# Performance work log

Measured on AMD Instinct MI355X. Metric: run time of the kernel, lower is better.

## Reference

```python
import jax, jax.numpy as jnp
import numpy as np

N_NODES = 50000
N_EDGES = 800000
D_IN = 128
D_OUT = 128
N_MLP = 2


def _lin(x, W, b):
    return x @ W.T + b


def setup_inputs() -> dict:
    key = jax.random.key(0)
    ks = jax.random.split(key, 32)
    d = {}
    d['feat'] = jax.random.normal(ks[0], (N_NODES, D_IN), dtype=jnp.float32)
    d['src'] = jax.random.randint(ks[1], (N_EDGES,), 0, N_NODES, dtype=jnp.int32)
    d['dst'] = jax.random.randint(ks[2], (N_EDGES,), 0, N_NODES, dtype=jnp.int32)
    s_in = 1.0 / np.sqrt(D_IN)
    s_out = 1.0 / np.sqrt(D_OUT)
    i = 3
    def w(shape, s):
        nonlocal i
        out = jax.random.normal(ks[i], shape, dtype=jnp.float32) * s
        i += 1
        return out
    for nm in ['asrc', 'adst', 'asub', 'amul']:
        d['W_' + nm] = w((D_OUT, D_IN), s_in)
        d['b_' + nm] = w((D_OUT,), s_in)
    d['W_aout'] = w((1, D_OUT), s_out)
    d['b_aout'] = w((1,), s_out)
    for nm in ['pool', 'pool2']:
        d['W_' + nm] = w((D_IN, D_IN), s_in)
        d['b_' + nm] = w((D_IN,), s_in)
    for nm in ['self', 'neigh', 'neigh2']:
        d['W_' + nm] = w((D_OUT, D_IN), s_in)
        d['b_' + nm] = w((D_OUT,), s_in)
    d['W_mlp'] = w((N_MLP, D_OUT, D_OUT), s_out)
    d['b_mlp'] = w((N_MLP, D_OUT), s_out)
    return d


def reference(feat, src, dst,
              W_asrc, b_asrc, W_adst, b_adst, W_asub, b_asub, W_amul, b_amul,
              W_aout, b_aout, W_pool, b_pool, W_pool2, b_pool2,
              W_self, b_self, W_neigh, b_neigh, W_neigh2, b_neigh2,
              W_mlp, b_mlp):
    gelu = lambda x: jax.nn.gelu(x, approximate=False)
    fs = feat[src]            # [E, D_IN] gathered source feats
    fd = feat[dst]            # [E, D_IN] gathered dest feats
    # edge attention score
    e = _lin(fs - fd, W_asub, b_asub) + _lin(fs * fd, W_amul, b_amul)
    e = e + _lin(feat, W_asrc, b_asrc)[src] + _lin(feat, W_adst, b_adst)[dst]
    e = gelu(e)
    e = jax.nn.leaky_relu(_lin(e, W_aout, b_aout), 0.2)  # [E, 1]
    deg = jax.ops.segment_sum(jnp.ones((src.shape[0],), jnp.float32), dst,
                              num_segments=N_NODES)      # in-degree
    has_in = (deg > 0)[:, None]
    # max-pool branch
    h = gelu(_lin(feat, W_pool, b_pool))
    m = e * h[src]
    neigh = jax.ops.segment_max(m, dst, num_segments=N_NODES)
    neigh = jnp.where(has_in, neigh, 0.0)
    # mean-pool branch
    h2 = gelu(_lin(feat, W_pool2, b_pool2))
    m2 = e * h2[src]
    neigh2 = jax.ops.segment_sum(m2, dst, num_segments=N_NODES)
    neigh2 = neigh2 / jnp.maximum(deg, 1.0)[:, None]
    rst = _lin(feat, W_self, b_self) + _lin(neigh, W_neigh, b_neigh) \
        + _lin(neigh2, W_neigh2, b_neigh2)
    for li in range(W_mlp.shape[0]):
        rst = rst + _lin(gelu(rst), W_mlp[li], b_mlp[li])
    return rst
```

## Files before the change

kernel.cpp:

```cpp
#include <hip/hip_runtime.h>
#include <cstdint>
#include <cstddef>

#define NN 50000
#define NE 800000
#define DD 128

static_assert(NN % 16 == 0, "node tiles");
static_assert(NE % 16 == 0, "edge tiles");

typedef __bf16 bf16_t;
typedef bf16_t bf16x8 __attribute__((ext_vector_type(8)));
typedef bf16_t bf16x4 __attribute__((ext_vector_type(4)));
typedef bf16_t bf16x2 __attribute__((ext_vector_type(2)));
typedef float f32x4 __attribute__((ext_vector_type(4)));
typedef float f32x16 __attribute__((ext_vector_type(16)));

__device__ __forceinline__ float gelu_f(float x) {
    float u = x * x;
    float t = fmaf(u, -0.1029442445f, -2.3021184019f);
    float s = __builtin_amdgcn_exp2f(x * t);
    return x * __builtin_amdgcn_rcpf(1.0f + s);
}

__device__ __forceinline__ int frag_idx(int ch, int k) {
    int t = ch >> 4, n = ch & 15;
    int kb = k >> 5, r = k & 31, q = r >> 3, j = r & 7;
    return ((((t * 4 + kb) * 4 + q) * 16 + n) << 3) + j;
}

__device__ __forceinline__ int frag32_idx(int ch, int k) {
    int t = ch >> 5, m = ch & 31;
    int kc = k >> 4, q = (k >> 3) & 1, j = k & 7;
    return ((((t * 8 + kc) * 2 + q) * 32 + m) << 3) + j;
}

__global__ __launch_bounds__(256) void convert_feat_kernel(
    const float* __restrict__ feat, bf16_t* __restrict__ fb,
    const int* __restrict__ dst, int* __restrict__ deg)
{
    int i = blockIdx.x * 256 + threadIdx.x;
    f32x4 v = ((const f32x4*)feat)[i];
    bf16x4 o;
    o[0] = (bf16_t)v[0]; o[1] = (bf16_t)v[1]; o[2] = (bf16_t)v[2]; o[3] = (bf16_t)v[3];
    ((bf16x4*)fb)[i] = o;
    if (i < NE) atomicAdd(&deg[dst[i]], 1);
}

__global__ __launch_bounds__(256) void prep_kernel(
    const float* __restrict__ W_asrc, const float* __restrict__ b_asrc,
    const float* __restrict__ W_adst, const float* __restrict__ b_adst,
    const float* __restrict__ W_asub, const float* __restrict__ b_asub,
    const float* __restrict__ W_amul, const float* __restrict__ b_amul,
    const float* __restrict__ W_pool, const float* __restrict__ W_pool2,
    const float* __restrict__ W_self, const float* __restrict__ b_self,
    const float* __restrict__ W_neigh, const float* __restrict__ b_neigh,
    const float* __restrict__ W_neigh2, const float* __restrict__ b_neigh2,
    const float* __restrict__ W_mlp,
    bf16_t* __restrict__ W_Sf, bf16_t* __restrict__ W_Df, bf16_t* __restrict__ W_amulf,
    bf16_t* __restrict__ W_poolf, bf16_t* __restrict__ W_pool2f,
    bf16_t* __restrict__ W_selff, bf16_t* __restrict__ W_neighf, bf16_t* __restrict__ W_neigh2f,
    bf16_t* __restrict__ W_mlpf,
    float* __restrict__ b_e, float* __restrict__ b_rst)
{
    int gid = blockIdx.x * 256 + threadIdx.x;
    float sub = W_asub[gid];
    int ch = gid >> 7, k = gid & 127;
    int fi = frag_idx(ch, k);
    W_Sf[fi] = (bf16_t)(W_asrc[gid] + sub);
    W_Df[fi] = (bf16_t)(W_adst[gid] - sub);
    W_amulf[frag32_idx(ch, k)] = (bf16_t)W_amul[gid];
    W_poolf[fi]   = (bf16_t)W_pool[gid];
    W_pool2f[fi]  = (bf16_t)W_pool2[gid];
    W_selff[fi]   = (bf16_t)W_self[gid];
    W_neighf[fi]  = (bf16_t)W_neigh[gid];
    W_neigh2f[fi] = (bf16_t)W_neigh2[gid];
    W_mlpf[fi]            = (bf16_t)W_mlp[gid];
    W_mlpf[DD * DD + fi]  = (bf16_t)W_mlp[DD * DD + gid];
    if (gid < DD) {
        b_e[gid]   = b_asub[gid] + b_amul[gid] + b_asrc[gid] + b_adst[gid];
        b_rst[gid] = b_self[gid] + b_neigh[gid] + b_neigh2[gid];
    }
}

__device__ __forceinline__ void mm16_store_ilv(
    const bf16x8 a[4], const bf16_t* __restrict__ Wf, const float* __restrict__ bias,
    bf16_t* __restrict__ hh, int nb, int n, int q, int lane, int sub)
{
#pragma unroll
    for (int t = 0; t < 8; t++) {
        f32x4 acc = {0.f, 0.f, 0.f, 0.f};
#pragma unroll
        for (int kb = 0; kb < 4; kb++) {
            bf16x8 b = *(const bf16x8*)(Wf + (((t * 4 + kb) * 64 + lane) << 3));
            acc = __builtin_amdgcn_mfma_f32_16x16x32_bf16(a[kb], b, acc, 0, 0, 0);
        }
        int ch = t * 16 + n;
        int pos = ((ch >> 1) << 2) + (ch & 1) + sub;
        float bv = bias[ch];
#pragma unroll
        for (int r = 0; r < 4; r++)
            hh[(size_t)(nb + q * 4 + r) * 256 + pos] = (bf16_t)gelu_f(acc[r] + bv);
    }
}

__device__ __forceinline__ void mm16_store_plain(
    const bf16x8 a[4], const bf16_t* __restrict__ Wf, const float* __restrict__ bias,
    bf16_t* __restrict__ out, int nb, int n, int q, int lane)
{
#pragma unroll
    for (int t = 0; t < 8; t++) {
        f32x4 acc = {0.f, 0.f, 0.f, 0.f};
#pragma unroll
        for (int kb = 0; kb < 4; kb++) {
            bf16x8 b = *(const bf16x8*)(Wf + (((t * 4 + kb) * 64 + lane) << 3));
            acc = __builtin_amdgcn_mfma_f32_16x16x32_bf16(a[kb], b, acc, 0, 0, 0);
        }
        int ch = t * 16 + n;
        float bv = bias ? bias[ch] : 0.0f;
#pragma unroll
        for (int r = 0; r < 4; r++)
            out[(size_t)(nb + q * 4 + r) * DD + ch] = (bf16_t)(acc[r] + bv);
    }
}

__global__ __launch_bounds__(256) void node_linear_kernel(
    const bf16_t* __restrict__ fb,
    const bf16_t* __restrict__ W_poolf, const float* __restrict__ b_pool,
    const bf16_t* __restrict__ W_pool2f, const float* __restrict__ b_pool2,
    const bf16_t* __restrict__ W_Sf, const float* __restrict__ b_e,
    const bf16_t* __restrict__ W_Df,
    bf16_t* __restrict__ hh, bf16_t* __restrict__ us, bf16_t* __restrict__ ud)
{
    int wid = blockIdx.x * 4 + (threadIdx.x >> 6);
    if (wid >= NN / 16) return;
    int lane = threadIdx.x & 63, n = lane & 15, q = lane >> 4;
    int nb = wid * 16;
    bf16x8 a[4];
#pragma unroll
    for (int kb = 0; kb < 4; kb++)
        a[kb] = *(const bf16x8*)(fb + (size_t)(nb + n) * DD + kb * 32 + q * 8);
    mm16_store_ilv(a, W_poolf, b_pool, hh, nb, n, q, lane, 0);
    mm16_store_ilv(a, W_pool2f, b_pool2, hh, nb, n, q, lane, 2);
    mm16_store_plain(a, W_Sf, b_e, us, nb, n, q, lane);
    mm16_store_plain(a, W_Df, nullptr, ud, nb, n, q, lane);
}

#define SCAN_NB ((NN + 255) / 256)

__global__ __launch_bounds__(256) void scan1_kernel(const int* __restrict__ deg,
                                                    int* __restrict__ offsets, int* __restrict__ bsum)
{
    __shared__ int tmp[256];
    int t = threadIdx.x, g = blockIdx.x * 256 + t;
    int v = (g < NN) ? deg[g] : 0;
    tmp[t] = v;
    __syncthreads();
#pragma unroll
    for (int d = 1; d < 256; d <<= 1) {
        int x = (t >= d) ? tmp[t - d] : 0;
        __syncthreads();
        tmp[t] += x;
        __syncthreads();
    }
    if (g < NN) offsets[g] = tmp[t] - v;
    if (t == 255) bsum[blockIdx.x] = tmp[255];
}

__global__ __launch_bounds__(256) void scan2_kernel(const int* __restrict__ bsum, int* __restrict__ bbase)
{
    __shared__ int tmp[256];
    int t = threadIdx.x;
    int v = (t < SCAN_NB) ? bsum[t] : 0;
    tmp[t] = v;
    __syncthreads();
#pragma unroll
    for (int d = 1; d < 256; d <<= 1) {
        int x = (t >= d) ? tmp[t - d] : 0;
        __syncthreads();
        tmp[t] += x;
        __syncthreads();
    }
    if (t < SCAN_NB) bbase[t] = tmp[t] - v;
}

__global__ __launch_bounds__(256) void scan3_kernel(const int* __restrict__ bbase,
                                                    int* __restrict__ offsets, int* __restrict__ cursor)
{
    int g = blockIdx.x * 256 + threadIdx.x;
    if (g < NN) {
        int o = offsets[g] + bbase[blockIdx.x];
        offsets[g] = o;
        cursor[g] = o;
    }
}

#define ES_NBLK 2500
#define ES_ITERS (NE / 32 / ES_NBLK)

__global__ __launch_bounds__(256, 4) void edge_score_kernel(
    const bf16_t* __restrict__ fb, const int* __restrict__ src, const int* __restrict__ dst,
    const bf16_t* __restrict__ us, const bf16_t* __restrict__ ud,
    const bf16_t* __restrict__ W_amulf,
    const float* __restrict__ w_aout, const float* __restrict__ b_aout,
    int* __restrict__ cursor, int2* __restrict__ csr)
{
    __shared__ __align__(16) bf16_t sP[2][32 * 128];
    __shared__ __align__(16) bf16_t sU[2][32 * 128];
    __shared__ float partials[32 * 5];
    __shared__ float sWa[128];
    int tid = threadIdx.x;
    int wave = tid >> 6, lane = tid & 63;
    int n = lane & 31, q = lane >> 5;
    int t = wave;

    if (tid < 128) sWa[tid] = w_aout[tid];

    bf16x8 wAm[8];
#pragma unroll
    for (int kc = 0; kc < 8; kc++)
        wAm[kc] = *(const bf16x8*)(W_amulf + ((((t * 8 + kc) * 2 + q) * 32 + n) << 3));
    float bout = b_aout[0];

    int sed0 = tid >> 4, sc = tid & 15;

    int e0 = blockIdx.x * 32;
    int s0 = src[e0 + sed0],      d0 = dst[e0 + sed0];
    int s1 = src[e0 + sed0 + 16], d1 = dst[e0 + sed0 + 16];
    bf16x8 pfs0 = *(const bf16x8*)(fb + (size_t)s0 * DD + sc * 8);
    bf16x8 pfd0 = *(const bf16x8*)(fb + (size_t)d0 * DD + sc * 8);
    bf16x8 pus0 = *(const bf16x8*)(us + (size_t)s0 * DD + sc * 8);
    bf16x8 pud0 = *(const bf16x8*)(ud + (size_t)d0 * DD + sc * 8);
    bf16x8 pfs1 = *(const bf16x8*)(fb + (size_t)s1 * DD + sc * 8);
    bf16x8 pfd1 = *(const bf16x8*)(fb + (size_t)d1 * DD + sc * 8);
    bf16x8 pus1 = *(const bf16x8*)(us + (size_t)s1 * DD + sc * 8);
    bf16x8 pud1 = *(const bf16x8*)(ud + (size_t)d1 * DD + sc * 8);

    for (int it = 0; it < ES_ITERS; it++) {
        int buf = it & 1;
        int eb = (blockIdx.x + it * ES_NBLK) * 32;
        {
            bf16x8 pp, uu;
#pragma unroll
            for (int j = 0; j < 8; j++) {
                pp[j] = (bf16_t)((float)pfs0[j] * (float)pfd0[j]);
                uu[j] = (bf16_t)((float)pus0[j] + (float)pud0[j]);
            }
            int ph = (sc ^ (sed0 & 7)) << 3;
            *(bf16x8*)(sP[buf] + sed0 * 128 + ph) = pp;
            *(bf16x8*)(sU[buf] + sed0 * 128 + ph) = uu;
        }
        {
            int ed = sed0 + 16;
            bf16x8 pp, uu;
#pragma unroll
            for (int j = 0; j < 8; j++) {
                pp[j] = (bf16_t)((float)pfs1[j] * (float)pfd1[j]);
                uu[j] = (bf16_t)((float)pus1[j] + (float)pud1[j]);
            }
            int ph = (sc ^ (ed & 7)) << 3;
            *(bf16x8*)(sP[buf] + ed * 128 + ph) = pp;
            *(bf16x8*)(sU[buf] + ed * 128 + ph) = uu;
        }
        __syncthreads();
        if (it + 1 < ES_ITERS) {
            int e1 = (blockIdx.x + (it + 1) * ES_NBLK) * 32;
            s0 = src[e1 + sed0];      d0 = dst[e1 + sed0];
            s1 = src[e1 + sed0 + 16]; d1 = dst[e1 + sed0 + 16];
            pfs0 = *(const bf16x8*)(fb + (size_t)s0 * DD + sc * 8);
            pfd0 = *(const bf16x8*)(fb + (size_t)d0 * DD + sc * 8);
            pus0 = *(const bf16x8*)(us + (size_t)s0 * DD + sc * 8);
            pud0 = *(const bf16x8*)(ud + (size_t)d0 * DD + sc * 8);
            pfs1 = *(const bf16x8*)(fb + (size_t)s1 * DD + sc * 8);
            pfd1 = *(const bf16x8*)(fb + (size_t)d1 * DD + sc * 8);
            pus1 = *(const bf16x8*)(us + (size_t)s1 * DD + sc * 8);
            pud1 = *(const bf16x8*)(ud + (size_t)d1 * DD + sc * 8);
        }
        f32x16 acc = {};
        int swz = n & 7;
#pragma unroll
        for (int kc = 0; kc < 8; kc++) {
            bf16x8 bP = *(const bf16x8*)(sP[buf] + n * 128 + (((kc * 2 + q) ^ swz) << 3));
            acc = __builtin_amdgcn_mfma_f32_32x32x16_bf16(wAm[kc], bP, acc, 0, 0, 0);
        }
        float psum = 0.f;
#pragma unroll
        for (int c = 0; c < 4; c++) {
            bf16x4 sv = *(const bf16x4*)(sU[buf] + n * 128 + (((t * 4 + c) ^ swz) << 3) + q * 4);
            f32x4 wv = *(const f32x4*)(sWa + t * 32 + c * 8 + q * 4);
#pragma unroll
            for (int j = 0; j < 4; j++)
                psum = fmaf(gelu_f(acc[c * 4 + j] + (float)sv[j]), wv[j], psum);
        }
        psum += __shfl_xor(psum, 32, 64);
        if (lane < 32) partials[lane * 5 + wave] = psum;
        __syncthreads();
        if (wave == (it & 3) && lane < 32) {
            int e = eb + lane;
            const float* pr = partials + lane * 5;
            float s = pr[0] + pr[1] + pr[2] + pr[3] + bout;
            s = s > 0.f ? s : 0.2f * s;
            int d = dst[e];
            int pos = atomicAdd(&cursor[d], 1);
            int2 pk;
            pk.x = src[e];
            pk.y = __float_as_int(s);
            csr[pos] = pk;
        }
    }
}

__global__ __launch_bounds__(256) void aggregate_kernel(
    const bf16_t* __restrict__ hh,
    const int* __restrict__ offsets, const int* __restrict__ cursor_end,
    const int2* __restrict__ csr,
    bf16_t* __restrict__ neigh, bf16_t* __restrict__ neigh2)
{
    int wave = threadIdx.x >> 6, lane = threadIdx.x & 63;
    int v = blockIdx.x * 4 + wave;
    if (v >= NN) return;
    int off = offsets[v];
    int dg = cursor_end[v] - off;
    int quarter = lane >> 4;
    int cl = lane & 15;
    float mx[8], sm[8];
#pragma unroll
    for (int j = 0; j < 8; j++) { mx[j] = -INFINITY; sm[j] = 0.f; }
    for (int base = 0; base < dg; base += 64) {
        int cnt = dg - base; if (cnt > 64) cnt = 64;
        int s_l = 0; float sc_l = 0.f;
        if (lane < cnt) {
            int2 pk = csr[off + base + lane];
            s_l = pk.x;
            sc_l = __int_as_float(pk.y);
        }
        int nit = (cnt + 3) >> 2;
#pragma unroll 2
        for (int i = 0; i < nit; i++) {
            int idx = 4 * i + quarter;
            int s = __shfl(s_l, idx, 64);
            float sc = __shfl(sc_l, idx, 64);
            if (idx < cnt) {
                const bf16_t* row = hh + (size_t)s * 256 + 16 * cl;
                bf16x8 h0 = *(const bf16x8*)(row);
                bf16x8 h1 = *(const bf16x8*)(row + 8);
                mx[0] = fmaxf(mx[0], sc * (float)h0[0]);
                mx[1] = fmaxf(mx[1], sc * (float)h0[1]);
                sm[0] = fmaf(sc, (float)h0[2], sm[0]);
                sm[1] = fmaf(sc, (float)h0[3], sm[1]);
                mx[2] = fmaxf(mx[2], sc * (float)h0[4]);
                mx[3] = fmaxf(mx[3], sc * (float)h0[5]);
                sm[2] = fmaf(sc, (float)h0[6], sm[2]);
                sm[3] = fmaf(sc, (float)h0[7], sm[3]);
                mx[4] = fmaxf(mx[4], sc * (float)h1[0]);
                mx[5] = fmaxf(mx[5], sc * (float)h1[1]);
                sm[4] = fmaf(sc, (float)h1[2], sm[4]);
                sm[5] = fmaf(sc, (float)h1[3], sm[5]);
                mx[6] = fmaxf(mx[6], sc * (float)h1[4]);
                mx[7] = fmaxf(mx[7], sc * (float)h1[5]);
                sm[6] = fmaf(sc, (float)h1[6], sm[6]);
                sm[7] = fmaf(sc, (float)h1[7], sm[7]);
            }
        }
    }
#pragma unroll
    for (int j = 0; j < 8; j++) {
        mx[j] = fmaxf(mx[j], __shfl_xor(mx[j], 16, 64));
        mx[j] = fmaxf(mx[j], __shfl_xor(mx[j], 32, 64));
        sm[j] += __shfl_xor(sm[j], 16, 64);
        sm[j] += __shfl_xor(sm[j], 32, 64);
    }
    if (quarter == 0) {
        float inv = 1.0f / (float)(dg > 1 ? dg : 1);
        bf16x8 n1, n2;
#pragma unroll
        for (int j = 0; j < 8; j++) {
            n1[j] = (bf16_t)(dg > 0 ? mx[j] : 0.0f);
            n2[j] = (bf16_t)(sm[j] * inv);
        }
        *(bf16x8*)(neigh + (size_t)v * DD + 8 * cl) = n1;
        *(bf16x8*)(neigh2 + (size_t)v * DD + 8 * cl) = n2;
    }
}

__global__ __launch_bounds__(256) void final_kernel(
    const bf16_t* __restrict__ fb, const bf16_t* __restrict__ neigh, const bf16_t* __restrict__ neigh2,
    const bf16_t* __restrict__ W_selff, const bf16_t* __restrict__ W_neighf, const bf16_t* __restrict__ W_neigh2f,
    const float* __restrict__ b_rst,
    const bf16_t* __restrict__ W_mlpf, const float* __restrict__ b_mlp,
    float* __restrict__ out)
{
    __shared__ __align__(16) float lds[4][16 * 132];
    int wave = threadIdx.x >> 6;
    int wid = blockIdx.x * 4 + wave;
    if (wid >= NN / 16) return;
    int lane = threadIdx.x & 63, n = lane & 15, q = lane >> 4;
    int nb = wid * 16;
    float* L = lds[wave];

    bf16x8 af[4], an[4], am[4];
#pragma unroll
    for (int kb = 0; kb < 4; kb++) {
        size_t o = (size_t)(nb + n) * DD + kb * 32 + q * 8;
        af[kb] = *(const bf16x8*)(fb + o);
        an[kb] = *(const bf16x8*)(neigh + o);
        am[kb] = *(const bf16x8*)(neigh2 + o);
    }
    f32x4 rst[8];
#pragma unroll
    for (int t = 0; t < 8; t++) {
        f32x4 acc = {0.f, 0.f, 0.f, 0.f};
#pragma unroll
        for (int kb = 0; kb < 4; kb++) {
            int wo = ((t * 4 + kb) * 64 + lane) << 3;
            acc = __builtin_amdgcn_mfma_f32_16x16x32_bf16(af[kb], *(const bf16x8*)(W_selff + wo), acc, 0, 0, 0);
            acc = __builtin_amdgcn_mfma_f32_16x16x32_bf16(an[kb], *(const bf16x8*)(W_neighf + wo), acc, 0, 0, 0);
            acc = __builtin_amdgcn_mfma_f32_16x16x32_bf16(am[kb], *(const bf16x8*)(W_neigh2f + wo), acc, 0, 0, 0);
        }
        float bv = b_rst[t * 16 + n];
#pragma unroll
        for (int r = 0; r < 4; r++) acc[r] += bv;
        rst[t] = acc;
    }

#pragma unroll
    for (int li = 0; li < 2; li++) {
#pragma unroll
        for (int t = 0; t < 8; t++)
#pragma unroll
            for (int r = 0; r < 4; r++)
                L[(q * 4 + r) * 132 + t * 16 + n] = gelu_f(rst[t][r]);
        __builtin_amdgcn_wave_barrier();
        bf16x8 g[4];
#pragma unroll
        for (int kb = 0; kb < 4; kb++) {
            const f32x4* p = (const f32x4*)&L[n * 132 + kb * 32 + q * 8];
            f32x4 x0 = p[0], x1 = p[1];
            bf16x8 gg;
            gg[0] = (bf16_t)x0[0]; gg[1] = (bf16_t)x0[1]; gg[2] = (bf16_t)x0[2]; gg[3] = (bf16_t)x0[3];
            gg[4] = (bf16_t)x1[0]; gg[5] = (bf16_t)x1[1]; gg[6] = (bf16_t)x1[2]; gg[7] = (bf16_t)x1[3];
            g[kb] = gg;
        }
        __builtin_amdgcn_wave_barrier();
        const bf16_t* Wl = W_mlpf + li * DD * DD;
#pragma unroll
        for (int t = 0; t < 8; t++) {
            f32x4 acc = {0.f, 0.f, 0.f, 0.f};
#pragma unroll
            for (int kb = 0; kb < 4; kb++) {
                bf16x8 b = *(const bf16x8*)(Wl + (((t * 4 + kb) * 64 + lane) << 3));
                acc = __builtin_amdgcn_mfma_f32_16x16x32_bf16(g[kb], b, acc, 0, 0, 0);
            }
            float bm = b_mlp[li * DD + t * 16 + n];
#pragma unroll
            for (int r = 0; r < 4; r++) rst[t][r] += acc[r] + bm;
        }
    }

#pragma unroll
    for (int t = 0; t < 8; t++)
#pragma unroll
        for (int r = 0; r < 4; r++)
            out[(size_t)(nb + q * 4 + r) * DD + t * 16 + n] = rst[t][r];
}

extern "C" void kernel_launch(void* const* d_in, const int* in_sizes, int n_in,
                              void* d_out, int out_size, void* d_ws, size_t ws_size,
                              hipStream_t stream)
{
    const float* feat    = (const float*)d_in[0];
    const int*   src     = (const int*)d_in[1];
    const int*   dst     = (const int*)d_in[2];
    const float* W_asrc  = (const float*)d_in[3],  *b_asrc  = (const float*)d_in[4];
    const float* W_adst  = (const float*)d_in[5],  *b_adst  = (const float*)d_in[6];
    const float* W_asub  = (const float*)d_in[7],  *b_asub  = (const float*)d_in[8];
    const float* W_amul  = (const float*)d_in[9],  *b_amul  = (const float*)d_in[10];
    const float* W_aout  = (const float*)d_in[11], *b_aout  = (const float*)d_in[12];
    const float* W_pool  = (const float*)d_in[13], *b_pool  = (const float*)d_in[14];
    const float* W_pool2 = (const float*)d_in[15], *b_pool2 = (const float*)d_in[16];
    const float* W_self  = (const float*)d_in[17], *b_self  = (const float*)d_in[18];
    const float* W_neigh = (const float*)d_in[19], *b_neigh = (const float*)d_in[20];
    const float* W_neigh2= (const float*)d_in[21], *b_neigh2= (const float*)d_in[22];
    const float* W_mlp   = (const float*)d_in[23], *b_mlp   = (const float*)d_in[24];
    float* out = (float*)d_out;

    char* w = (char*)d_ws;
    auto take = [&](size_t bytes) -> void* {
        void* p = (void*)w;
        w += (bytes + 255) & ~(size_t)255;
        return p;
    };
    bf16_t* fb      = (bf16_t*)take((size_t)NN * DD * sizeof(bf16_t));
    bf16_t* neigh   = (bf16_t*)take((size_t)NN * DD * sizeof(bf16_t));
    bf16_t* neigh2  = (bf16_t*)take((size_t)NN * DD * sizeof(bf16_t));
    bf16_t* hh      = (bf16_t*)take((size_t)NN * 256 * sizeof(bf16_t));
    bf16_t* us      = (bf16_t*)take((size_t)NN * DD * sizeof(bf16_t));
    bf16_t* ud      = (bf16_t*)take((size_t)NN * DD * sizeof(bf16_t));
    int*    deg     = (int*)take((size_t)NN * sizeof(int));
    int*    offsets = (int*)take((size_t)NN * sizeof(int));
    int*    cursor  = (int*)take((size_t)NN * sizeof(int));
    int2*   csr     = (int2*)take((size_t)NE * sizeof(int2));
    int*    bsum    = (int*)take(256 * sizeof(int));
    int*    bbase   = (int*)take(256 * sizeof(int));
    bf16_t* W_Sf    = (bf16_t*)take((size_t)DD * DD * sizeof(bf16_t));
    bf16_t* W_Df    = (bf16_t*)take((size_t)DD * DD * sizeof(bf16_t));
    bf16_t* W_amulf = (bf16_t*)take((size_t)DD * DD * sizeof(bf16_t));
    bf16_t* W_poolf = (bf16_t*)take((size_t)DD * DD * sizeof(bf16_t));
    bf16_t* W_pool2f= (bf16_t*)take((size_t)DD * DD * sizeof(bf16_t));
    bf16_t* W_selff = (bf16_t*)take((size_t)DD * DD * sizeof(bf16_t));
    bf16_t* W_neighf= (bf16_t*)take((size_t)DD * DD * sizeof(bf16_t));
    bf16_t* W_neigh2f=(bf16_t*)take((size_t)DD * DD * sizeof(bf16_t));
    bf16_t* W_mlpf  = (bf16_t*)take((size_t)2 * DD * DD * sizeof(bf16_t));
    float*  b_e     = (float*)take((size_t)DD * sizeof(float));
    float*  b_rst   = (float*)take((size_t)DD * sizeof(float));

    (void)hipMemsetAsync(deg, 0, (size_t)NN * sizeof(int), stream);

    convert_feat_kernel<<<NN * DD / 4 / 256, 256, 0, stream>>>(feat, fb, dst, deg);

    prep_kernel<<<DD * DD / 256, 256, 0, stream>>>(
        W_asrc, b_asrc, W_adst, b_adst, W_asub, b_asub, W_amul, b_amul,
        W_pool, W_pool2, W_self, b_self, W_neigh, b_neigh, W_neigh2, b_neigh2, W_mlp,
        W_Sf, W_Df, W_amulf, W_poolf, W_pool2f, W_selff, W_neighf, W_neigh2f, W_mlpf,
        b_e, b_rst);

    const int nwaves = NN / 16;
    const int ngrid = (nwaves + 3) / 4;
    node_linear_kernel<<<ngrid, 256, 0, stream>>>(
        fb, W_poolf, b_pool, W_pool2f, b_pool2, W_Sf, b_e, W_Df, hh, us, ud);

    scan1_kernel<<<SCAN_NB, 256, 0, stream>>>(deg, offsets, bsum);
    scan2_kernel<<<1, 256, 0, stream>>>(bsum, bbase);
    scan3_kernel<<<SCAN_NB, 256, 0, stream>>>(bbase, offsets, cursor);

    edge_score_kernel<<<ES_NBLK, 256, 0, stream>>>(
        fb, src, dst, us, ud, W_amulf, W_aout, b_aout, cursor, csr);

    aggregate_kernel<<<(NN + 3) / 4, 256, 0, stream>>>(
        hh, offsets, cursor, csr, neigh, neigh2);

    final_kernel<<<ngrid, 256, 0, stream>>>(
        fb, neigh, neigh2, W_selff, W_neighf, W_neigh2f, b_rst, W_mlpf, b_mlp, out);
}
```

Before: 425.8 us.

## Sort edges by destination before scoring so edge gathers hit dst-sorted order

```diff
diff --git a/kernel.cpp b/kernel.cpp
--- a/kernel.cpp
+++ b/kernel.cpp
@@ -195,15 +195,30 @@
     }
 }
 
+__global__ __launch_bounds__(256) void reorder_kernel(
+    const int* __restrict__ src, const int* __restrict__ dst,
+    int* __restrict__ cursor, int2* __restrict__ csr)
+{
+    int e = blockIdx.x * 256 + threadIdx.x;
+    if (e < NE) {
+        int d = dst[e];
+        int pos = atomicAdd(&cursor[d], 1);
+        int2 pk;
+        pk.x = src[e];
+        pk.y = d;
+        csr[pos] = pk;
+    }
+}
+
 #define ES_NBLK 2500
 #define ES_ITERS (NE / 32 / ES_NBLK)
 
 __global__ __launch_bounds__(256, 4) void edge_score_kernel(
-    const bf16_t* __restrict__ fb, const int* __restrict__ src, const int* __restrict__ dst,
+    const bf16_t* __restrict__ fb,
     const bf16_t* __restrict__ us, const bf16_t* __restrict__ ud,
     const bf16_t* __restrict__ W_amulf,
     const float* __restrict__ w_aout, const float* __restrict__ b_aout,
-    int* __restrict__ cursor, int2* __restrict__ csr)
+    int2* __restrict__ csr)
 {
     __shared__ __align__(16) bf16_t sP[2][32 * 128];
     __shared__ __align__(16) bf16_t sU[2][32 * 128];
@@ -225,16 +240,16 @@
     int sed0 = tid >> 4, sc = tid & 15;
 
     int e0 = blockIdx.x * 32;
-    int s0 = src[e0 + sed0],      d0 = dst[e0 + sed0];
-    int s1 = src[e0 + sed0 + 16], d1 = dst[e0 + sed0 + 16];
-    bf16x8 pfs0 = *(const bf16x8*)(fb + (size_t)s0 * DD + sc * 8);
-    bf16x8 pfd0 = *(const bf16x8*)(fb + (size_t)d0 * DD + sc * 8);
-    bf16x8 pus0 = *(const bf16x8*)(us + (size_t)s0 * DD + sc * 8);
-    bf16x8 pud0 = *(const bf16x8*)(ud + (size_t)d0 * DD + sc * 8);
-    bf16x8 pfs1 = *(const bf16x8*)(fb + (size_t)s1 * DD + sc * 8);
-    bf16x8 pfd1 = *(const bf16x8*)(fb + (size_t)d1 * DD + sc * 8);
-    bf16x8 pus1 = *(const bf16x8*)(us + (size_t)s1 * DD + sc * 8);
-    bf16x8 pud1 = *(const bf16x8*)(ud + (size_t)d1 * DD + sc * 8);
+    int2 pk0 = csr[e0 + sed0];
+    int2 pk1 = csr[e0 + sed0 + 16];
+    bf16x8 pfs0 = *(const bf16x8*)(fb + (size_t)pk0.x * DD + sc * 8);
+    bf16x8 pfd0 = *(const bf16x8*)(fb + (size_t)pk0.y * DD + sc * 8);
+    bf16x8 pus0 = *(const bf16x8*)(us + (size_t)pk0.x * DD + sc * 8);
+    bf16x8 pud0 = *(const bf16x8*)(ud + (size_t)pk0.y * DD + sc * 8);
+    bf16x8 pfs1 = *(const bf16x8*)(fb + (size_t)pk1.x * DD + sc * 8);
+    bf16x8 pfd1 = *(const bf16x8*)(fb + (size_t)pk1.y * DD + sc * 8);
+    bf16x8 pus1 = *(const bf16x8*)(us + (size_t)pk1.x * DD + sc * 8);
+    bf16x8 pud1 = *(const bf16x8*)(ud + (size_t)pk1.y * DD + sc * 8);
 
     for (int it = 0; it < ES_ITERS; it++) {
         int buf = it & 1;
@@ -265,16 +280,16 @@
         __syncthreads();
         if (it + 1 < ES_ITERS) {
             int e1 = (blockIdx.x + (it + 1) * ES_NBLK) * 32;
-            s0 = src[e1 + sed0];      d0 = dst[e1 + sed0];
-            s1 = src[e1 + sed0 + 16]; d1 = dst[e1 + sed0 + 16];
-            pfs0 = *(const bf16x8*)(fb + (size_t)s0 * DD + sc * 8);
-            pfd0 = *(const bf16x8*)(fb + (size_t)d0 * DD + sc * 8);
-            pus0 = *(const bf16x8*)(us + (size_t)s0 * DD + sc * 8);
-            pud0 = *(const bf16x8*)(ud + (size_t)d0 * DD + sc * 8);
-            pfs1 = *(const bf16x8*)(fb + (size_t)s1 * DD + sc * 8);
-            pfd1 = *(const bf16x8*)(fb + (size_t)d1 * DD + sc * 8);
-            pus1 = *(const bf16x8*)(us + (size_t)s1 * DD + sc * 8);
-            pud1 = *(const bf16x8*)(ud + (size_t)d1 * DD + sc * 8);
+            pk0 = csr[e1 + sed0];
+            pk1 = csr[e1 + sed0 + 16];
+            pfs0 = *(const bf16x8*)(fb + (size_t)pk0.x * DD + sc * 8);
+            pfd0 = *(const bf16x8*)(fb + (size_t)pk0.y * DD + sc * 8);
+            pus0 = *(const bf16x8*)(us + (size_t)pk0.x * DD + sc * 8);
+            pud0 = *(const bf16x8*)(ud + (size_t)pk0.y * DD + sc * 8);
+            pfs1 = *(const bf16x8*)(fb + (size_t)pk1.x * DD + sc * 8);
+            pfd1 = *(const bf16x8*)(fb + (size_t)pk1.y * DD + sc * 8);
+            pus1 = *(const bf16x8*)(us + (size_t)pk1.x * DD + sc * 8);
+            pud1 = *(const bf16x8*)(ud + (size_t)pk1.y * DD + sc * 8);
         }
         f32x16 acc = {};
         int swz = n & 7;
@@ -296,23 +311,17 @@
         if (lane < 32) partials[lane * 5 + wave] = psum;
         __syncthreads();
         if (wave == (it & 3) && lane < 32) {
-            int e = eb + lane;
             const float* pr = partials + lane * 5;
             float s = pr[0] + pr[1] + pr[2] + pr[3] + bout;
             s = s > 0.f ? s : 0.2f * s;
-            int d = dst[e];
-            int pos = atomicAdd(&cursor[d], 1);
-            int2 pk;
-            pk.x = src[e];
-            pk.y = __float_as_int(s);
-            csr[pos] = pk;
+            csr[eb + lane].y = __float_as_int(s);
         }
     }
 }
 
 __global__ __launch_bounds__(256) void aggregate_kernel(
     const bf16_t* __restrict__ hh,
-    const int* __restrict__ offsets, const int* __restrict__ cursor_end,
+    const int* __restrict__ offsets, const int* __restrict__ deg,
     const int2* __restrict__ csr,
     bf16_t* __restrict__ neigh, bf16_t* __restrict__ neigh2)
 {
@@ -320,7 +329,7 @@
     int v = blockIdx.x * 4 + wave;
     if (v >= NN) return;
     int off = offsets[v];
-    int dg = cursor_end[v] - off;
+    int dg = deg[v];
     int quarter = lane >> 4;
     int cl = lane & 15;
     float mx[8], sm[8];
@@ -524,20 +533,22 @@
         W_Sf, W_Df, W_amulf, W_poolf, W_pool2f, W_selff, W_neighf, W_neigh2f, W_mlpf,
         b_e, b_rst);
 
+    scan1_kernel<<<SCAN_NB, 256, 0, stream>>>(deg, offsets, bsum);
+    scan2_kernel<<<1, 256, 0, stream>>>(bsum, bbase);
+    scan3_kernel<<<SCAN_NB, 256, 0, stream>>>(bbase, offsets, cursor);
+
+    reorder_kernel<<<(NE + 255) / 256, 256, 0, stream>>>(src, dst, cursor, csr);
+
     const int nwaves = NN / 16;
     const int ngrid = (nwaves + 3) / 4;
     node_linear_kernel<<<ngrid, 256, 0, stream>>>(
         fb, W_poolf, b_pool, W_pool2f, b_pool2, W_Sf, b_e, W_Df, hh, us, ud);
 
-    scan1_kernel<<<SCAN_NB, 256, 0, stream>>>(deg, offsets, bsum);
-    scan2_kernel<<<1, 256, 0, stream>>>(bsum, bbase);
-    scan3_kernel<<<SCAN_NB, 256, 0, stream>>>(bbase, offsets, cursor);
-
     edge_score_kernel<<<ES_NBLK, 256, 0, stream>>>(
-        fb, src, dst, us, ud, W_amulf, W_aout, b_aout, cursor, csr);
+        fb, us, ud, W_amulf, W_aout, b_aout, csr);
 
     aggregate_kernel<<<(NN + 3) / 4, 256, 0, stream>>>(
-        hh, offsets, cursor, csr, neigh, neigh2);
+        hh, offsets, deg, csr, neigh, neigh2);
 
     final_kernel<<<ngrid, 256, 0, stream>>>(
         fb, neigh, neigh2, W_selff, W_neighf, W_neigh2f, b_rst, W_mlpf, b_mlp, out);
```

After: 433.0 us. Within noise of the previous version (+1.7%).
